# Kernel tuning notes

Hardware: AMD Instinct MI355X
Metric: run time of the kernel (lower is better)

Reference implementation:

```python
import jax, jax.numpy as jnp
import numpy as np
from jax import lax

B, T, V, E, H = 8, 512, 32000, 256, 512
NEG = -1e9


def setup_inputs() -> dict:
    key = jax.random.key(0)
    ks = jax.random.split(key, 13)
    g = lambda k, shp, sc: (jax.random.normal(k, shp, jnp.float32) * sc)
    return {
        'x': jax.random.randint(ks[0], (B, T), 0, V),
        'lengths': jax.random.randint(ks[1], (B,), T // 2, T + 1),
        'embed': g(ks[2], (V, E), 0.02),
        'W_ih': g(ks[3], (H, E), 1.0 / np.sqrt(E)),
        'W_hh': g(ks[4], (H, H), 1.0 / np.sqrt(H)),
        'b_ih': g(ks[5], (H,), 0.01),
        'b_hh': g(ks[6], (H,), 0.01),
        'attn_W': g(ks[7], (H, 2 * H), 1.0 / np.sqrt(2 * H)),
        'attn_b': g(ks[8], (H,), 0.01),
        'attn_v': g(ks[9], (1, H), 1.0 / np.sqrt(H)),
        'attn_v_b': g(ks[10], (1,), 0.01),
        'fc_W': g(ks[11], (V, 2 * H), 1.0 / np.sqrt(2 * H)),
        'fc_b': g(ks[12], (V,), 0.01),
    }


def reference(x, lengths, embed, W_ih, W_hh, b_ih, b_hh,
              attn_W, attn_b, attn_v, attn_v_b, fc_W, fc_b):
    b, t = x.shape
    h = W_ih.shape[0]
    # embedding with padding_idx=0 (row 0 forced to zero)
    tab = embed.at[0].set(0.0)
    emb = tab[x]  # [B,T,E]
    # vanilla tanh RNN via scan (precompute input projection)
    xin = emb @ W_ih.T + b_ih  # [B,T,H]

    def rnn_step(hprev, xt):
        hnew = jnp.tanh(xt + hprev @ W_hh.T + b_hh)
        return hnew, hnew

    _, out = lax.scan(rnn_step, jnp.zeros((b, h), xin.dtype), xin.transpose(1, 0, 2))
    out = out.transpose(1, 0, 2)  # [B,T,H]
    # pad_packed_sequence zeros hidden states past each sequence length
    len_mask = jnp.arange(t)[None, :] < lengths[:, None]  # [B,T]
    out = out * len_mask[..., None].astype(out.dtype)

    # additive attention: score(t,s) = v . tanh(W1 h_t + W2 h_s + b)
    W1, W2 = attn_W[:, :h], attn_W[:, h:]
    q = out @ W1.T            # [B,T,H]
    k = out @ W2.T + attn_b   # [B,T,H]
    v = attn_v[0]             # [H]

    def att_row(_, qt):  # qt: [B,H] -> scores over all s: [B,T]
        s = jnp.tanh(qt[:, None, :] + k) @ v + attn_v_b[0]
        return None, s

    _, scores = lax.scan(att_row, None, q.transpose(1, 0, 2))  # [T,B,T]
    scores = scores.transpose(1, 0, 2)  # [B,T(query),T(key)]
    causal = jnp.arange(t)[:, None] >= jnp.arange(t)[None, :]  # s <= t
    valid = causal[None] & len_mask[:, None, :]
    scores = jnp.where(valid, scores, NEG)
    alpha = jax.nn.softmax(scores, axis=-1)
    context = jnp.einsum('bts,bsh->bth', alpha, out)  # [B,T,H]
    feats = jnp.concatenate([out, context], axis=-1)  # [B,T,2H]
    logits = feats @ fc_W.T + fc_b  # [B,T,V]
    return logits
```

## Files before the change

### kernel.cpp

```cpp
#include <hip/hip_runtime.h>
#include <hip/hip_bf16.h>

typedef __attribute__((ext_vector_type(8))) short short8;
typedef __attribute__((ext_vector_type(4))) float f32x4;
typedef __attribute__((ext_vector_type(4))) unsigned int u32x4;

__device__ __forceinline__ void glds16(const void* g, void* l) {
  __builtin_amdgcn_global_load_lds(
      (const __attribute__((address_space(1))) unsigned int*)g,
      (__attribute__((address_space(3))) unsigned int*)l, 16, 0, 0);
}

__device__ __forceinline__ void bar_lds() {
  asm volatile("s_waitcnt lgkmcnt(0)\n\ts_barrier" ::: "memory");
}

__device__ __forceinline__ float fast_tanh(float x) {
  float e = __expf(2.0f * x);
  return (e - 1.0f) * __builtin_amdgcn_rcpf(e + 1.0f);
}

__device__ __forceinline__ unsigned short bfh(float f) {
  __hip_bfloat16 h = __float2bfloat16(f);
  return *reinterpret_cast<unsigned short*>(&h);
}
__device__ __forceinline__ float bf2f(unsigned short u) {
  unsigned v = ((unsigned)u) << 16;
  float f;
  __builtin_memcpy(&f, &v, 4);
  return f;
}
__device__ __forceinline__ short bf16r(float f) { return (short)bfh(f); }

union FragU {
  unsigned int u[4];
  short8 s;
};

__global__ __launch_bounds__(256) void k_xin(const int* __restrict__ x, const float* __restrict__ embed,
                                             const float* __restrict__ W_ih, const float* __restrict__ b_ih,
                                             float* __restrict__ xin) {
  __shared__ float At[64][128];
  __shared__ float Bt[128][64];
  const int tid = threadIdx.x;
  const int bt0 = blockIdx.x * 64, j0 = blockIdx.y * 64;
  const int ty = tid >> 4, tx = tid & 15;
  const int lane = tid & 63, cgrp = tid >> 6;
  float acc[4][4] = {};
  for (int kc = 0; kc < 256; kc += 128) {
#pragma unroll
    for (int rr = 0; rr < 8; ++rr) {
      int row = rr * 8 + (tid >> 5);
      int col = (tid & 31) * 4;
      int tok = x[bt0 + row];
      float4 v = make_float4(0.f, 0.f, 0.f, 0.f);
      if (tok != 0) v = *(const float4*)&embed[(size_t)tok * 256 + kc + col];
      *(float4*)&At[row][col] = v;
    }
#pragma unroll
    for (int cc = 0; cc < 8; ++cc) {
      int col = cgrp * 32 + cc * 4;
      float4 v = *(const float4*)&W_ih[(size_t)(j0 + lane) * 256 + kc + col];
      Bt[col + 0][lane] = v.x; Bt[col + 1][lane] = v.y;
      Bt[col + 2][lane] = v.z; Bt[col + 3][lane] = v.w;
    }
    __syncthreads();
    for (int kk = 0; kk < 128; ++kk) {
      float bv[4];
#pragma unroll
      for (int c = 0; c < 4; ++c) bv[c] = Bt[kk][tx * 4 + c];
#pragma unroll
      for (int a = 0; a < 4; ++a) {
        float av = At[ty * 4 + a][kk];
#pragma unroll
        for (int c = 0; c < 4; ++c) acc[a][c] = fmaf(av, bv[c], acc[a][c]);
      }
    }
    __syncthreads();
  }
#pragma unroll
  for (int a = 0; a < 4; ++a) {
    int m = bt0 + ty * 4 + a;
#pragma unroll
    for (int c = 0; c < 4; ++c) {
      int j = j0 + tx * 4 + c;
      xin[(size_t)m * 512 + j] = acc[a][c] + b_ih[j];
    }
  }
}

__global__ __launch_bounds__(512) void k_rnn(const float* __restrict__ xin, const float* __restrict__ W_hh,
                                             const float* __restrict__ b_hh, const int* __restrict__ lengths,
                                             unsigned long long* mbox, float* __restrict__ out,
                                             unsigned short* __restrict__ feats,
                                             const float* __restrict__ fcW, unsigned short* __restrict__ fcWb) {
  const int tid = threadIdx.x;
  if (blockIdx.x >= 8) {
    const size_t stride = (size_t)(gridDim.x - 8) * 512 * 8;
    for (size_t i = ((size_t)(blockIdx.x - 8) * 512 + tid) * 8; i < 32768000ull; i += stride) {
      float4 a = *(const float4*)(fcW + i);
      float4 b = *(const float4*)(fcW + i + 4);
      short8 v;
      v[0] = bf16r(a.x); v[1] = bf16r(a.y); v[2] = bf16r(a.z); v[3] = bf16r(a.w);
      v[4] = bf16r(b.x); v[5] = bf16r(b.y); v[6] = bf16r(b.z); v[7] = bf16r(b.w);
      *(short8*)(fcWb + i) = v;
    }
    return;
  }
  const int blk = blockIdx.x;
  const int w = tid >> 6, l = tid & 63;
  const int jt = w & 3, kh = w >> 2;
  const int j16 = blk * 64 + jt * 16;
  const int r = l & 15;
  const int g = l >> 4;
  const int n = l & 15;

  __shared__ unsigned long long stg[2048];
  __shared__ f32x4 Cbuf[4][64];
  __shared__ float hLf[8][64];
  __shared__ unsigned int hL32[8][64];

  short8 bhi[8], blo[8];
  {
    const float* wrow = &W_hh[(size_t)(j16 + n) * 512];
#pragma unroll
    for (int c8 = 0; c8 < 8; ++c8) {
      int c = kh * 8 + c8;
      const float* wp = wrow + c * 32 + g * 8;
      float4 wa = *(const float4*)wp;
      float4 wb = *(const float4*)(wp + 4);
      float wv[8] = {wa.x, wa.y, wa.z, wa.w, wb.x, wb.y, wb.z, wb.w};
#pragma unroll
      for (int e = 0; e < 8; ++e) {
        unsigned short h = bfh(wv[e]);
        bhi[c8][e] = (short)h;
        blo[c8][e] = (short)bfh(wv[e] - bf2f(h));
      }
    }
  }

  float bj = 0.f, xv[4];
  if (w < 4 && l < 32) {
    bj = b_hh[j16 + n];
#pragma unroll
    for (int i = 0; i < 4; ++i)
      xv[i] = xin[((size_t)(g * 4 + i) * 512 + 0) * 512 + j16 + n];
  }
  const int mylen = lengths[(tid >> 6) & 7];

  __syncthreads();

  const int sgran = tid ^ ((tid >> 6) & 3);

  for (int t = 0; t < 512; ++t) {
    unsigned long long* slotp = mbox + ((size_t)blk * 16 + (t & 15)) * 2048 + tid * 4;
    {
      u32x4 A, B2;
      int guard = 0;
      while (true) {
        asm volatile(
            "global_load_dwordx4 %0, %2, off sc0 sc1\n\t"
            "global_load_dwordx4 %1, %2, off offset:16 sc0 sc1\n\t"
            "s_waitcnt vmcnt(0)"
            : "=&v"(A), "=&v"(B2)
            : "v"(slotp)
            : "memory");
        bool ok = true;
#pragma unroll
        for (int q = 0; q < 4; ++q) ok = ok && (A[q] != 0xFFFFFFFFu) && (B2[q] != 0xFFFFFFFFu);
        if (ok || ++guard == (1 << 20)) break;
      }
      stg[sgran * 4 + 0] = (unsigned long long)A[0] | ((unsigned long long)A[1] << 32);
      stg[sgran * 4 + 1] = (unsigned long long)A[2] | ((unsigned long long)A[3] << 32);
      stg[sgran * 4 + 2] = (unsigned long long)B2[0] | ((unsigned long long)B2[1] << 32);
      stg[sgran * 4 + 3] = (unsigned long long)B2[2] | ((unsigned long long)B2[3] << 32);
      bar_lds();
    }

    f32x4 acc0 = {}, acc1 = {};
#pragma unroll
    for (int c8 = 0; c8 < 8; ++c8) {
      FragU ah, al;
      if (r < 8) {
        int gran = r * 64 + kh * 32 + c8 * 4 + g;
        int gs = (gran ^ (r & 3)) * 4;
        unsigned long long u0 = stg[gs + 0], u1 = stg[gs + 1];
        unsigned long long u2 = stg[gs + 2], u3 = stg[gs + 3];
        ah.u[0] = (unsigned)u0; al.u[0] = (unsigned)(u0 >> 32);
        ah.u[1] = (unsigned)u1; al.u[1] = (unsigned)(u1 >> 32);
        ah.u[2] = (unsigned)u2; al.u[2] = (unsigned)(u2 >> 32);
        ah.u[3] = (unsigned)u3; al.u[3] = (unsigned)(u3 >> 32);
      } else {
        ah.u[0] = ah.u[1] = ah.u[2] = ah.u[3] = 0u;
        al.u[0] = al.u[1] = al.u[2] = al.u[3] = 0u;
      }
      if (c8 & 1) {
        acc1 = __builtin_amdgcn_mfma_f32_16x16x32_bf16(ah.s, bhi[c8], acc1, 0, 0, 0);
        acc1 = __builtin_amdgcn_mfma_f32_16x16x32_bf16(ah.s, blo[c8], acc1, 0, 0, 0);
        acc1 = __builtin_amdgcn_mfma_f32_16x16x32_bf16(al.s, bhi[c8], acc1, 0, 0, 0);
      } else {
        acc0 = __builtin_amdgcn_mfma_f32_16x16x32_bf16(ah.s, bhi[c8], acc0, 0, 0, 0);
        acc0 = __builtin_amdgcn_mfma_f32_16x16x32_bf16(ah.s, blo[c8], acc0, 0, 0, 0);
        acc0 = __builtin_amdgcn_mfma_f32_16x16x32_bf16(al.s, bhi[c8], acc0, 0, 0, 0);
      }
    }
    f32x4 tot = acc0 + acc1;

    if (w >= 4) Cbuf[w - 4][l] = tot;
    bar_lds();
    if (w < 4) {
      tot += Cbuf[w][l];
      if (l < 32) {
#pragma unroll
        for (int i = 0; i < 4; ++i) {
          int b = g * 4 + i;
          float hn = fast_tanh(xv[i] + tot[i] + bj);
          hLf[b][jt * 16 + n] = hn;
          unsigned hi = bfh(hn);
          unsigned lo = bfh(hn - bf2f((unsigned short)hi));
          hL32[b][jt * 16 + n] = hi | (lo << 16);
        }
        int tt = (t < 511) ? t + 1 : 511;
#pragma unroll
        for (int i = 0; i < 4; ++i)
          xv[i] = xin[((size_t)(g * 4 + i) * 512 + tt) * 512 + j16 + n];
      }
    }
    bar_lds();

    if (t < 511) {
      unsigned long long* dst = mbox + ((size_t)w * 16 + ((t + 1) & 15)) * 2048 + blk * 32;
      const int e0 = (l & 15) * 4;
#pragma unroll
      for (int k2 = 0; k2 < 2; ++k2) {
        int b = (l >> 4) + k2 * 4;
        unsigned a0 = hL32[b][e0 + 0], a1 = hL32[b][e0 + 1];
        unsigned a2 = hL32[b][e0 + 2], a3 = hL32[b][e0 + 3];
        u32x4 val;
        val[0] = (a0 & 0xffffu) | (a1 << 16);
        val[1] = (a0 >> 16) | (a1 & 0xffff0000u);
        val[2] = (a2 & 0xffffu) | (a3 << 16);
        val[3] = (a2 >> 16) | (a3 & 0xffff0000u);
        unsigned long long* p = dst + (size_t)b * 256 + (l & 15) * 2;
        asm volatile("global_store_dwordx4 %0, %1, off sc0 sc1" :: "v"(p), "v"(val) : "memory");
      }
      u32x4 S;
      S[0] = S[1] = S[2] = S[3] = 0xFFFFFFFFu;
      asm volatile(
          "global_store_dwordx4 %0, %1, off sc0 sc1\n\t"
          "global_store_dwordx4 %0, %1, off offset:16 sc0 sc1"
          :: "v"(slotp), "v"(S)
          : "memory");
    }
    {
      int b = tid >> 6, jl = tid & 63;
      float hv = hLf[b][jl];
      hv = (t < mylen) ? hv : 0.f;
      out[((size_t)b * 512 + t) * 512 + blk * 64 + jl] = hv;
      feats[((size_t)b * 512 + t) * 1024 + blk * 64 + jl] = bfh(hv);
    }
  }
}

__global__ __launch_bounds__(256) void k_qk(const float* __restrict__ out, const float* __restrict__ attn_W,
                                            const float* __restrict__ attn_b, float* __restrict__ qdst,
                                            float* __restrict__ kdst) {
  __shared__ float At[64][128];
  __shared__ float Bt[128][64];
  const int tid = threadIdx.x;
  const int MODE = blockIdx.z;
  const int bt0 = blockIdx.x * 64, j0 = blockIdx.y * 64;
  const int ty = tid >> 4, tx = tid & 15;
  const int lane = tid & 63, cgrp = tid >> 6;
  float acc[4][4] = {};
  for (int kc = 0; kc < 512; kc += 128) {
#pragma unroll
    for (int rr = 0; rr < 8; ++rr) {
      int row = rr * 8 + (tid >> 5);
      int col = (tid & 31) * 4;
      *(float4*)&At[row][col] = *(const float4*)&out[((size_t)bt0 + row) * 512 + kc + col];
    }
#pragma unroll
    for (int cc = 0; cc < 8; ++cc) {
      int col = cgrp * 32 + cc * 4;
      float4 v = *(const float4*)&attn_W[(size_t)(j0 + lane) * 1024 + (MODE ? 512 : 0) + kc + col];
      Bt[col + 0][lane] = v.x; Bt[col + 1][lane] = v.y;
      Bt[col + 2][lane] = v.z; Bt[col + 3][lane] = v.w;
    }
    __syncthreads();
    for (int kk = 0; kk < 128; ++kk) {
      float bv[4];
#pragma unroll
      for (int c = 0; c < 4; ++c) bv[c] = Bt[kk][tx * 4 + c];
#pragma unroll
      for (int a = 0; a < 4; ++a) {
        float av = At[ty * 4 + a][kk];
#pragma unroll
        for (int c = 0; c < 4; ++c) acc[a][c] = fmaf(av, bv[c], acc[a][c]);
      }
    }
    __syncthreads();
  }
#pragma unroll
  for (int a = 0; a < 4; ++a) {
    int bt = bt0 + ty * 4 + a;
#pragma unroll
    for (int c = 0; c < 4; ++c) {
      int j = j0 + tx * 4 + c;
      if (MODE == 0) {
        qdst[(size_t)bt * 512 + j] = acc[a][c];
      } else {
        int bb = bt >> 9, tt = bt & 511;
        kdst[((size_t)bb * 512 + j) * 512 + tt] = acc[a][c] + attn_b[j];
      }
    }
  }
}

__global__ __launch_bounds__(256) void k_scores(const float* __restrict__ q, const float* __restrict__ kT,
                                                const float* __restrict__ attn_v, const float* __restrict__ attn_v_b,
                                                const int* __restrict__ lengths, float* __restrict__ pbuf,
                                                float* __restrict__ invl) {
  const int b = blockIdx.x, t0 = blockIdx.y * 4;
  const int tid = threadIdx.x;
  __shared__ float qL[4][512];
  __shared__ float vL[512];
  __shared__ float red[4][4];
  for (int i = tid; i < 4 * 512; i += 256) {
    int rr = i >> 9, h = i & 511;
    qL[rr][h] = q[((size_t)b * 512 + t0 + rr) * 512 + h];
  }
  for (int i = tid; i < 512; i += 256) vL[i] = attn_v[i];
  const float vb = attn_v_b[0];
  const int len = lengths[b];
  __syncthreads();
  const int s_hi = min(t0 + 3, len - 1);
  const float* kTb = kT + (size_t)b * 512 * 512;
  float psum[4] = {0.f, 0.f, 0.f, 0.f};
#pragma unroll
  for (int si = 0; si < 2; ++si) {
    int s = tid + si * 256;
    float acc[4] = {0.f, 0.f, 0.f, 0.f};
    if (s <= s_hi) {
      for (int h = 0; h < 512; ++h) {
        float kv = kTb[(size_t)h * 512 + s];
        float vh = vL[h];
#pragma unroll
        for (int rr = 0; rr < 4; ++rr) acc[rr] = fmaf(vh, fast_tanh(qL[rr][h] + kv), acc[rr]);
      }
    }
#pragma unroll
    for (int rr = 0; rr < 4; ++rr) {
      int t = t0 + rr;
      bool valid = (s <= t) && (s < len);
      float p = valid ? __expf(acc[rr] + vb - 20.f) : 0.f;
      pbuf[((size_t)b * 512 + t) * 512 + s] = p;
      psum[rr] += p;
    }
  }
  const int wv = tid >> 6, ln = tid & 63;
#pragma unroll
  for (int rr = 0; rr < 4; ++rr) {
    float v = psum[rr];
#pragma unroll
    for (int m = 1; m < 64; m <<= 1) v += __shfl_xor(v, m);
    if (ln == 0) red[wv][rr] = v;
  }
  __syncthreads();
  if (tid < 4) {
    float s = red[0][tid] + red[1][tid] + red[2][tid] + red[3][tid];
    invl[(size_t)b * 512 + t0 + tid] = 1.0f / s;
  }
}

__global__ __launch_bounds__(256) void k_context(const float* __restrict__ pbuf, const float* __restrict__ out,
                                                 const float* __restrict__ invl, unsigned short* __restrict__ feats) {
  __shared__ float Pt[64][128];
  __shared__ float Ot[128][64];
  const int b = blockIdx.z, t0 = blockIdx.y * 64, h0 = blockIdx.x * 64;
  const int tid = threadIdx.x, ty = tid >> 4, tx = tid & 15;
  float acc[4][4] = {};
  for (int sc = 0; sc < 512; sc += 128) {
#pragma unroll
    for (int rr = 0; rr < 8; ++rr) {
      int row = rr * 8 + (tid >> 5);
      int col = (tid & 31) * 4;
      *(float4*)&Pt[row][col] = *(const float4*)&pbuf[((size_t)b * 512 + t0 + row) * 512 + sc + col];
    }
#pragma unroll
    for (int rr = 0; rr < 8; ++rr) {
      int srow = rr * 16 + (tid >> 4);
      int col = (tid & 15) * 4;
      *(float4*)&Ot[srow][col] = *(const float4*)&out[((size_t)b * 512 + sc + srow) * 512 + h0 + col];
    }
    __syncthreads();
    for (int kk = 0; kk < 128; ++kk) {
      float ov[4];
#pragma unroll
      for (int c = 0; c < 4; ++c) ov[c] = Ot[kk][tx * 4 + c];
#pragma unroll
      for (int a = 0; a < 4; ++a) {
        float pv = Pt[ty * 4 + a][kk];
#pragma unroll
        for (int c = 0; c < 4; ++c) acc[a][c] = fmaf(pv, ov[c], acc[a][c]);
      }
    }
    __syncthreads();
  }
#pragma unroll
  for (int a = 0; a < 4; ++a) {
    int t = t0 + ty * 4 + a;
    float il = invl[b * 512 + t];
#pragma unroll
    for (int c = 0; c < 4; ++c) {
      int h = h0 + tx * 4 + c;
      feats[((size_t)b * 512 + t) * 1024 + 512 + h] = (unsigned short)bf16r(acc[a][c] * il);
    }
  }
}

__global__ __launch_bounds__(256) void k_logits(const unsigned short* __restrict__ A,
                                                const unsigned short* __restrict__ Bw,
                                                const float* __restrict__ bias, float* __restrict__ C) {
  const int linb = blockIdx.x;
  const int xcd = linb & 7, pos = linb >> 3;
  const int m0 = (xcd * 4 + (pos & 3)) * 128;
  const int n0 = (pos >> 2) * 128;
  __shared__ unsigned short As[128 * 64];
  __shared__ unsigned short Bs[128 * 64];
  const int tid = threadIdx.x;
  const int wave = tid >> 6, lane = tid & 63;
  const int wm = (wave >> 1) * 64, wn = (wave & 1) * 64;
  const int lo16 = lane & 15, oct = lane >> 4;
  f32x4 acc[4][4] = {};
  for (int kt = 0; kt < 1024; kt += 64) {
#pragma unroll
    for (int i = 0; i < 4; ++i) {
      int ci = wave * 4 + i;
      int mrow = ci * 8 + (lane >> 3);
      int k8 = (lane & 7) * 8;
      glds16(&A[(size_t)(m0 + mrow) * 1024 + kt + k8], &As[ci * 512]);
      glds16(&Bw[(size_t)(n0 + mrow) * 1024 + kt + k8], &Bs[ci * 512]);
    }
    __syncthreads();
#pragma unroll
    for (int kk = 0; kk < 2; ++kk) {
      short8 af[4], bf[4];
#pragma unroll
      for (int i = 0; i < 4; ++i)
        af[i] = *(const short8*)&As[(wm + i * 16 + lo16) * 64 + kk * 32 + oct * 8];
#pragma unroll
      for (int jn = 0; jn < 4; ++jn)
        bf[jn] = *(const short8*)&Bs[(wn + jn * 16 + lo16) * 64 + kk * 32 + oct * 8];
#pragma unroll
      for (int i = 0; i < 4; ++i)
#pragma unroll
        for (int jn = 0; jn < 4; ++jn)
          acc[i][jn] = __builtin_amdgcn_mfma_f32_16x16x32_bf16(af[i], bf[jn], acc[i][jn], 0, 0, 0);
    }
    __syncthreads();
  }
#pragma unroll
  for (int jn = 0; jn < 4; ++jn) {
    int nn = n0 + wn + jn * 16 + lo16;
    float bv = bias[nn];
#pragma unroll
    for (int i = 0; i < 4; ++i) {
      int mbase = m0 + wm + i * 16 + oct * 4;
#pragma unroll
      for (int rr = 0; rr < 4; ++rr)
        C[(size_t)(mbase + rr) * 32000 + nn] = acc[i][jn][rr] + bv;
    }
  }
}

extern "C" void kernel_launch(void* const* d_in, const int* in_sizes, int n_in,
                              void* d_out, int out_size, void* d_ws, size_t ws_size,
                              hipStream_t stream) {
  const int* x = (const int*)d_in[0];
  const int* lengths = (const int*)d_in[1];
  const float* embed = (const float*)d_in[2];
  const float* W_ih = (const float*)d_in[3];
  const float* W_hh = (const float*)d_in[4];
  const float* b_ih = (const float*)d_in[5];
  const float* b_hh = (const float*)d_in[6];
  const float* attn_W = (const float*)d_in[7];
  const float* attn_b = (const float*)d_in[8];
  const float* attn_v = (const float*)d_in[9];
  const float* attn_v_b = (const float*)d_in[10];
  const float* fc_W = (const float*)d_in[11];
  const float* fc_b = (const float*)d_in[12];
  float* logits = (float*)d_out;

  char* ws = (char*)d_ws;
  const size_t MB8 = 8388608;
  float* xin  = (float*)(ws);
  float* outp = (float*)(ws + 1 * MB8);
  float* q    = (float*)(ws + 2 * MB8);
  float* kT   = (float*)(ws + 3 * MB8);
  float* pbuf = (float*)(ws + 4 * MB8);
  float* invl = (float*)(ws + 5 * MB8);
  unsigned short* feats = (unsigned short*)(ws + 5 * MB8 + 16384);
  unsigned short* fcWb  = (unsigned short*)(ws + 6 * MB8 + 16384);
  unsigned long long* mbox = (unsigned long long*)pbuf;

  hipMemsetAsync(mbox, 0xFF, 8 * 16 * 16384, stream);
  for (int d = 0; d < 8; ++d)
    hipMemsetAsync((char*)mbox + (size_t)d * 16 * 16384, 0x00, 16384, stream);
  k_xin<<<dim3(64, 8), 256, 0, stream>>>(x, embed, W_ih, b_ih, xin);
  k_rnn<<<136, 512, 0, stream>>>(xin, W_hh, b_hh, lengths, mbox, outp, feats, fc_W, fcWb);
  k_qk<<<dim3(64, 8, 2), 256, 0, stream>>>(outp, attn_W, attn_b, q, kT);
  k_scores<<<dim3(8, 128), 256, 0, stream>>>(q, kT, attn_v, attn_v_b, lengths, pbuf, invl);
  k_context<<<dim3(8, 8, 8), 256, 0, stream>>>(pbuf, outp, invl, feats);
  k_logits<<<8000, 256, 0, stream>>>(feats, fcWb, fc_b, logits);
}
```

Measured before the change: 2.277 ms.

## Split the recurrent RNN across four blocks instead of eight, removing intra-block K split

The persistent RNN recurrence now runs on 4 cooperating blocks, each owning 128 hidden units, instead of 8 blocks with 64 units. Each wave covers the full K=512 reduction with 16 register-held W_hh fragments, so the per-step LDS partial-sum exchange and its extra barrier go away. Fewer blocks means less cross-block mailbox traffic and fewer participants in each step's global sync, at the cost of more MFMA work and register pressure per wave. Mailbox writes now broadcast to 4 destinations, the slot reset is spread over half the threads, and the out/feats stores are vectorised.

```diff
diff --git a/kernel.cpp b/kernel.cpp
--- a/kernel.cpp
+++ b/kernel.cpp
@@ -95,9 +95,9 @@
                                              unsigned short* __restrict__ feats,
                                              const float* __restrict__ fcW, unsigned short* __restrict__ fcWb) {
   const int tid = threadIdx.x;
-  if (blockIdx.x >= 8) {
-    const size_t stride = (size_t)(gridDim.x - 8) * 512 * 8;
-    for (size_t i = ((size_t)(blockIdx.x - 8) * 512 + tid) * 8; i < 32768000ull; i += stride) {
+  if (blockIdx.x >= 4) {
+    const size_t stride = (size_t)(gridDim.x - 4) * 512 * 8;
+    for (size_t i = ((size_t)(blockIdx.x - 4) * 512 + tid) * 8; i < 32768000ull; i += stride) {
       float4 a = *(const float4*)(fcW + i);
       float4 b = *(const float4*)(fcW + i + 4);
       short8 v;
@@ -109,23 +109,20 @@
   }
   const int blk = blockIdx.x;
   const int w = tid >> 6, l = tid & 63;
-  const int jt = w & 3, kh = w >> 2;
-  const int j16 = blk * 64 + jt * 16;
+  const int j16 = blk * 128 + w * 16;
   const int r = l & 15;
   const int g = l >> 4;
   const int n = l & 15;
 
   __shared__ unsigned long long stg[2048];
-  __shared__ f32x4 Cbuf[4][64];
-  __shared__ float hLf[8][64];
-  __shared__ unsigned int hL32[8][64];
-
-  short8 bhi[8], blo[8];
+  __shared__ float hLf[8][128];
+  __shared__ unsigned int hL32[8][128];
+
+  short8 bhi[16], blo[16];
   {
     const float* wrow = &W_hh[(size_t)(j16 + n) * 512];
 #pragma unroll
-    for (int c8 = 0; c8 < 8; ++c8) {
-      int c = kh * 8 + c8;
+    for (int c = 0; c < 16; ++c) {
       const float* wp = wrow + c * 32 + g * 8;
       float4 wa = *(const float4*)wp;
       float4 wb = *(const float4*)(wp + 4);
@@ -133,20 +130,20 @@
 #pragma unroll
       for (int e = 0; e < 8; ++e) {
         unsigned short h = bfh(wv[e]);
-        bhi[c8][e] = (short)h;
-        blo[c8][e] = (short)bfh(wv[e] - bf2f(h));
+        bhi[c][e] = (short)h;
+        blo[c][e] = (short)bfh(wv[e] - bf2f(h));
       }
     }
   }
 
   float bj = 0.f, xv[4];
-  if (w < 4 && l < 32) {
+  if (l < 32) {
     bj = b_hh[j16 + n];
 #pragma unroll
     for (int i = 0; i < 4; ++i)
       xv[i] = xin[((size_t)(g * 4 + i) * 512 + 0) * 512 + j16 + n];
   }
-  const int mylen = lengths[(tid >> 6) & 7];
+  const int mylen = lengths[tid >> 6];
 
   __syncthreads();
 
@@ -177,12 +174,12 @@
       bar_lds();
     }
 
-    f32x4 acc0 = {}, acc1 = {};
-#pragma unroll
-    for (int c8 = 0; c8 < 8; ++c8) {
+    f32x4 acc0 = {}, acc1 = {}, acc2 = {}, acc3 = {};
+#pragma unroll
+    for (int c = 0; c < 16; ++c) {
       FragU ah, al;
       if (r < 8) {
-        int gran = r * 64 + kh * 32 + c8 * 4 + g;
+        int gran = r * 64 + c * 4 + g;
         int gs = (gran ^ (r & 3)) * 4;
         unsigned long long u0 = stg[gs + 0], u1 = stg[gs + 1];
         unsigned long long u2 = stg[gs + 2], u3 = stg[gs + 3];
@@ -194,70 +191,82 @@
         ah.u[0] = ah.u[1] = ah.u[2] = ah.u[3] = 0u;
         al.u[0] = al.u[1] = al.u[2] = al.u[3] = 0u;
       }
-      if (c8 & 1) {
-        acc1 = __builtin_amdgcn_mfma_f32_16x16x32_bf16(ah.s, bhi[c8], acc1, 0, 0, 0);
-        acc1 = __builtin_amdgcn_mfma_f32_16x16x32_bf16(ah.s, blo[c8], acc1, 0, 0, 0);
-        acc1 = __builtin_amdgcn_mfma_f32_16x16x32_bf16(al.s, bhi[c8], acc1, 0, 0, 0);
+      if ((c & 3) == 0) {
+        acc0 = __builtin_amdgcn_mfma_f32_16x16x32_bf16(ah.s, bhi[c], acc0, 0, 0, 0);
+        acc0 = __builtin_amdgcn_mfma_f32_16x16x32_bf16(ah.s, blo[c], acc0, 0, 0, 0);
+        acc0 = __builtin_amdgcn_mfma_f32_16x16x32_bf16(al.s, bhi[c], acc0, 0, 0, 0);
+      } else if ((c & 3) == 1) {
+        acc1 = __builtin_amdgcn_mfma_f32_16x16x32_bf16(ah.s, bhi[c], acc1, 0, 0, 0);
+        acc1 = __builtin_amdgcn_mfma_f32_16x16x32_bf16(ah.s, blo[c], acc1, 0, 0, 0);
+        acc1 = __builtin_amdgcn_mfma_f32_16x16x32_bf16(al.s, bhi[c], acc1, 0, 0, 0);
+      } else if ((c & 3) == 2) {
+        acc2 = __builtin_amdgcn_mfma_f32_16x16x32_bf16(ah.s, bhi[c], acc2, 0, 0, 0);
+        acc2 = __builtin_amdgcn_mfma_f32_16x16x32_bf16(ah.s, blo[c], acc2, 0, 0, 0);
+        acc2 = __builtin_amdgcn_mfma_f32_16x16x32_bf16(al.s, bhi[c], acc2, 0, 0, 0);
       } else {
-        acc0 = __builtin_amdgcn_mfma_f32_16x16x32_bf16(ah.s, bhi[c8], acc0, 0, 0, 0);
-        acc0 = __builtin_amdgcn_mfma_f32_16x16x32_bf16(ah.s, blo[c8], acc0, 0, 0, 0);
-        acc0 = __builtin_amdgcn_mfma_f32_16x16x32_bf16(al.s, bhi[c8], acc0, 0, 0, 0);
-      }
-    }
-    f32x4 tot = acc0 + acc1;
-
-    if (w >= 4) Cbuf[w - 4][l] = tot;
+        acc3 = __builtin_amdgcn_mfma_f32_16x16x32_bf16(ah.s, bhi[c], acc3, 0, 0, 0);
+        acc3 = __builtin_amdgcn_mfma_f32_16x16x32_bf16(ah.s, blo[c], acc3, 0, 0, 0);
+        acc3 = __builtin_amdgcn_mfma_f32_16x16x32_bf16(al.s, bhi[c], acc3, 0, 0, 0);
+      }
+    }
+    f32x4 tot = (acc0 + acc1) + (acc2 + acc3);
+
+    if (l < 32) {
+#pragma unroll
+      for (int i = 0; i < 4; ++i) {
+        int b = g * 4 + i;
+        float hn = fast_tanh(xv[i] + tot[i] + bj);
+        hLf[b][w * 16 + n] = hn;
+        unsigned hi = bfh(hn);
+        unsigned lo = bfh(hn - bf2f((unsigned short)hi));
+        hL32[b][w * 16 + n] = hi | (lo << 16);
+      }
+      int tt = (t < 511) ? t + 1 : 511;
+#pragma unroll
+      for (int i = 0; i < 4; ++i)
+        xv[i] = xin[((size_t)(g * 4 + i) * 512 + tt) * 512 + j16 + n];
+    }
     bar_lds();
-    if (w < 4) {
-      tot += Cbuf[w][l];
-      if (l < 32) {
-#pragma unroll
-        for (int i = 0; i < 4; ++i) {
-          int b = g * 4 + i;
-          float hn = fast_tanh(xv[i] + tot[i] + bj);
-          hLf[b][jt * 16 + n] = hn;
-          unsigned hi = bfh(hn);
-          unsigned lo = bfh(hn - bf2f((unsigned short)hi));
-          hL32[b][jt * 16 + n] = hi | (lo << 16);
-        }
-        int tt = (t < 511) ? t + 1 : 511;
-#pragma unroll
-        for (int i = 0; i < 4; ++i)
-          xv[i] = xin[((size_t)(g * 4 + i) * 512 + tt) * 512 + j16 + n];
-      }
-    }
-    bar_lds();
 
     if (t < 511) {
-      unsigned long long* dst = mbox + ((size_t)w * 16 + ((t + 1) & 15)) * 2048 + blk * 32;
-      const int e0 = (l & 15) * 4;
-#pragma unroll
-      for (int k2 = 0; k2 < 2; ++k2) {
-        int b = (l >> 4) + k2 * 4;
-        unsigned a0 = hL32[b][e0 + 0], a1 = hL32[b][e0 + 1];
-        unsigned a2 = hL32[b][e0 + 2], a3 = hL32[b][e0 + 3];
+      if (tid < 256) {
+        int b = tid >> 5, jp0 = (tid & 31) * 2;
+        int jl = jp0 * 2;
+        unsigned a0 = hL32[b][jl + 0], a1 = hL32[b][jl + 1];
+        unsigned a2 = hL32[b][jl + 2], a3 = hL32[b][jl + 3];
         u32x4 val;
         val[0] = (a0 & 0xffffu) | (a1 << 16);
         val[1] = (a0 >> 16) | (a1 & 0xffff0000u);
         val[2] = (a2 & 0xffffu) | (a3 << 16);
         val[3] = (a2 >> 16) | (a3 & 0xffff0000u);
-        unsigned long long* p = dst + (size_t)b * 256 + (l & 15) * 2;
-        asm volatile("global_store_dwordx4 %0, %1, off sc0 sc1" :: "v"(p), "v"(val) : "memory");
-      }
-      u32x4 S;
-      S[0] = S[1] = S[2] = S[3] = 0xFFFFFFFFu;
-      asm volatile(
-          "global_store_dwordx4 %0, %1, off sc0 sc1\n\t"
-          "global_store_dwordx4 %0, %1, off offset:16 sc0 sc1"
-          :: "v"(slotp), "v"(S)
-          : "memory");
+        const size_t word = (size_t)b * 256 + blk * 64 + jp0;
+        const size_t slot = (size_t)((t + 1) & 15);
+#pragma unroll
+        for (int d = 0; d < 4; ++d) {
+          unsigned long long* p = mbox + ((size_t)d * 16 + slot) * 2048 + word;
+          asm volatile("global_store_dwordx4 %0, %1, off sc0 sc1" :: "v"(p), "v"(val) : "memory");
+        }
+      } else {
+        unsigned long long* rs = mbox + ((size_t)blk * 16 + (t & 15)) * 2048 + (size_t)(tid - 256) * 8;
+        u32x4 S;
+        S[0] = S[1] = S[2] = S[3] = 0xFFFFFFFFu;
+        asm volatile(
+            "global_store_dwordx4 %0, %1, off sc0 sc1\n\t"
+            "global_store_dwordx4 %0, %1, off offset:16 sc0 sc1\n\t"
+            "global_store_dwordx4 %0, %1, off offset:32 sc0 sc1\n\t"
+            "global_store_dwordx4 %0, %1, off offset:48 sc0 sc1"
+            :: "v"(rs), "v"(S)
+            : "memory");
+      }
     }
     {
-      int b = tid >> 6, jl = tid & 63;
-      float hv = hLf[b][jl];
-      hv = (t < mylen) ? hv : 0.f;
-      out[((size_t)b * 512 + t) * 512 + blk * 64 + jl] = hv;
-      feats[((size_t)b * 512 + t) * 1024 + blk * 64 + jl] = bfh(hv);
+      int b = tid >> 6, jl = (tid & 63) * 2;
+      float hv0 = hLf[b][jl], hv1 = hLf[b][jl + 1];
+      if (t >= mylen) { hv0 = 0.f; hv1 = 0.f; }
+      float2 f2 = make_float2(hv0, hv1);
+      *(float2*)&out[((size_t)b * 512 + t) * 512 + blk * 128 + jl] = f2;
+      unsigned pk = (unsigned)bfh(hv0) | ((unsigned)bfh(hv1) << 16);
+      *(unsigned*)&feats[((size_t)b * 512 + t) * 1024 + blk * 128 + jl] = pk;
     }
   }
 }
@@ -504,11 +513,11 @@
   unsigned short* fcWb  = (unsigned short*)(ws + 6 * MB8 + 16384);
   unsigned long long* mbox = (unsigned long long*)pbuf;
 
-  hipMemsetAsync(mbox, 0xFF, 8 * 16 * 16384, stream);
-  for (int d = 0; d < 8; ++d)
+  hipMemsetAsync(mbox, 0xFF, 4 * 16 * 16384, stream);
+  for (int d = 0; d < 4; ++d)
     hipMemsetAsync((char*)mbox + (size_t)d * 16 * 16384, 0x00, 16384, stream);
   k_xin<<<dim3(64, 8), 256, 0, stream>>>(x, embed, W_ih, b_ih, xin);
-  k_rnn<<<136, 512, 0, stream>>>(xin, W_hh, b_hh, lengths, mbox, outp, feats, fc_W, fcWb);
+  k_rnn<<<132, 512, 0, stream>>>(xin, W_hh, b_hh, lengths, mbox, outp, feats, fc_W, fcWb);
   k_qk<<<dim3(64, 8, 2), 256, 0, stream>>>(outp, attn_W, attn_b, q, kT);
   k_scores<<<dim3(8, 128), 256, 0, stream>>>(q, kT, attn_v, attn_v_b, lengths, pbuf, invl);
   k_context<<<dim3(8, 8, 8), 256, 0, stream>>>(pbuf, outp, invl, feats);
```

New measurement: 2.747 ms. 1.21x slower.
